# Kernel optimization log

Hardware: AMD Instinct MI355X
Metric: run time of the kernel (lower is better)

## Reference

```python
import jax, jax.numpy as jnp
import numpy as np

BLANK = 127
NEG = -1e30  # effective -inf that stays finite in fp32 arithmetic


def setup_inputs() -> dict:
    key = jax.random.key(0)
    k1, k2 = jax.random.split(key)
    outputs = jax.random.normal(k1, (64, 2048, 128), dtype=jnp.float32)
    # labels in [0, 127) -> never equal to blank (127)
    targets = jax.random.randint(k2, (64, 128), 0, BLANK)
    return {"outputs": outputs, "targets": targets}


def _ctc_loss(outputs, targets):
    # outputs: [B, T, V] logits, targets: [B, S] int labels (no blanks inside)
    B, T, V = outputs.shape
    S = targets.shape[1]
    L = 2 * S + 1  # extended label sequence length (blanks interleaved)

    log_probs = jax.nn.log_softmax(outputs, axis=2)  # [B, T, V]

    # extended labels: blank, y1, blank, y2, ..., blank
    ext = jnp.full((B, L), BLANK, dtype=targets.dtype)
    ext = ext.at[:, 1::2].set(targets)  # [B, L]

    # skip transition (l-2 -> l) allowed iff ext[l] != blank and ext[l] != ext[l-2]
    skip = jnp.concatenate(
        [jnp.zeros((B, 2), dtype=bool),
         (ext[:, 2:] != BLANK) & (ext[:, 2:] != ext[:, :-2])],
        axis=1,
    )  # [B, L]

    # gather per-step log-probs of extended labels: [B, T, L] -> [T, B, L]
    lp_ext = jnp.take_along_axis(log_probs, ext[:, None, :], axis=2)
    lp_ext = jnp.swapaxes(lp_ext, 0, 1)

    # alpha init at t=0: only states 0 (blank) and 1 (first label) reachable
    alpha0 = jnp.full((B, L), NEG, dtype=log_probs.dtype)
    alpha0 = alpha0.at[:, 0].set(lp_ext[0, :, 0])
    alpha0 = alpha0.at[:, 1].set(lp_ext[0, :, 1])

    neg1 = jnp.full((B, 1), NEG, dtype=log_probs.dtype)
    neg2 = jnp.full((B, 2), NEG, dtype=log_probs.dtype)

    def step(alpha, lp):
        s1 = jnp.concatenate([neg1, alpha[:, :-1]], axis=1)
        s2 = jnp.concatenate([neg2, alpha[:, :-2]], axis=1)
        s2 = jnp.where(skip, s2, NEG)
        alpha = lp + jnp.logaddexp(jnp.logaddexp(alpha, s1), s2)
        return alpha, None

    alphaT, _ = jax.lax.scan(step, alpha0, lp_ext[1:])

    # P(targets | outputs) ends in last blank or last label
    loss_b = -jnp.logaddexp(alphaT[:, L - 1], alphaT[:, L - 2])  # [B]

    # zero_infinity=True: unreachable paths -> zero loss
    loss_b = jnp.where(loss_b > 1e29, 0.0, loss_b)

    # reduction='mean': divide each loss by its target length, then batch-mean
    tl = jnp.sum(targets != BLANK, axis=1).astype(loss_b.dtype)
    return jnp.mean(loss_b / jnp.maximum(tl, 1.0))


def reference(outputs, targets):
    return _ctc_loss(outputs, targets)
```

## Files before the change

kernel.cpp:

```cpp
#include <hip/hip_runtime.h>
#include <stdint.h>


#define B_ 64
#define T_ 2048
#define V_ 128
#define S_ 128
#define BLANK 127
#define NCH 512
#define DEPTH 32
#define INFLT 28

__device__ __forceinline__ void glds16(const void* gsrc, void* lds) {
  __builtin_amdgcn_global_load_lds(
      (const __attribute__((address_space(1))) uint32_t*)gsrc,
      (__attribute__((address_space(3))) uint32_t*)lds, 16, 0, 0);
}

__global__ __launch_bounds__(256) void lse_kernel(const float* __restrict__ outp,
                                                  float2* __restrict__ lse2) {
  const float L2E = 1.4426950408889634f;
  int gtid = blockIdx.x * 256 + threadIdx.x;
  int wave = gtid >> 6;
  int lane = threadIdx.x & 63;
  long row = (long)wave * 2 + (lane >> 5);
  const float4 x = *(const float4*)(outp + row * V_ + (long)(lane & 31) * 4);
  float ex = exp2f(x.x * L2E), ey = exp2f(x.y * L2E);
  float ez = exp2f(x.z * L2E), ew = exp2f(x.w * L2E);
  float s = (ex + ey) + (ez + ew);
#pragma unroll
  for (int o = 1; o <= 16; o <<= 1) s += __shfl_xor(s, o);
  float bx = __shfl(x.w, (lane < 32) ? 31 : 63);
  if ((lane & 31) == 0) {
    float l2s = log2f(s);
    lse2[row] = make_float2(l2s, exp2f(fmaf(bx, L2E, -l2s)));
  }
}

__global__ __launch_bounds__(64) void ctc_alpha(const float* __restrict__ x,
                                                const float2* __restrict__ lse2,
                                                const int* __restrict__ tgt,
                                                float* __restrict__ lossb) {
  __shared__ __align__(16) float2 lp_s[T_];
  __shared__ __align__(16) float ring[DEPTH * 512];
  const float L2E = 1.4426950408889634f;
  const int b = blockIdx.x;
  const int k = threadIdx.x;

  const int2 tg = ((const int2*)(tgt + b * S_))[k];
  const int t1p = __shfl_up(tg.y, 1);
  const bool skip0 = (k > 0) && (tg.x != t1p);
  const bool skip1 = (tg.y != tg.x);
  const int tl = __popcll(__ballot(tg.x != BLANK)) + __popcll(__ballot(tg.y != BLANK));

  const float* lpsrc = (const float*)(lse2 + (long)b * T_);
#pragma unroll
  for (int i = 0; i < 16; ++i)
    glds16(lpsrc + i * 256 + k * 4, (float*)lp_s + i * 256);
  const float* xb = x + (long)b * T_ * V_;
  for (int i = 0; i < INFLT; ++i) {
    glds16(xb + i * 512 + k * 4, &ring[i * 512]);
    glds16(xb + i * 512 + 256 + k * 4, &ring[i * 512 + 256]);
  }
  asm volatile("s_waitcnt vmcnt(0)" ::: "memory");
  __builtin_amdgcn_sched_barrier(0);

  float fx0 = ring[0 * 128 + tg.x], fy0 = ring[0 * 128 + tg.y];
  float fx1 = ring[1 * 128 + tg.x], fy1 = ring[1 * 128 + tg.y];
  float fx2 = ring[2 * 128 + tg.x], fy2 = ring[2 * 128 + tg.y];
  float fx3 = ring[3 * 128 + tg.x], fy3 = ring[3 * 128 + tg.y];
  float2 lq0 = lp_s[0], lq1 = lp_s[1], lq2 = lp_s[2], lq3 = lp_s[3];

  float a0 = 0.f, a1 = 0.f, a2 = 0.f, a3 = 0.f, a4 = 0.f;
  float adj = 1.0f;
  int P = 0;

#define SUBSTEP(FX, FY, LQ) do {                                    \
    float p0 = exp2f(fmaf((FX), L2E, -(LQ).x));                     \
    float p1 = exp2f(fmaf((FY), L2E, -(LQ).x));                     \
    float pB = (LQ).y;                                              \
    float s1r = __shfl_up(a3, 1);                                   \
    float s1v = (k == 0) ? 0.f : s1r * adj;                         \
    float na0 = pB * (a0 + s1v);                                    \
    float na1 = p0 * (a1 + a0 + (skip0 ? s1v : 0.f));               \
    float na2 = pB * (a2 + a1);                                     \
    float na3 = p1 * (a3 + a2 + (skip1 ? a1 : 0.f));                \
    float na4 = pB * (a4 + a3);                                     \
    a4 = (k == 63) ? na4 : 0.f;                                     \
    a0 = na0; a1 = na1; a2 = na2; a3 = na3;                         \
  } while (0)

  int ws = INFLT % DEPTH, cn = INFLT;
  for (int c = 0; c < NCH; ++c) {
    glds16(xb + (long)cn * 512 + k * 4, &ring[ws * 512]);
    glds16(xb + (long)cn * 512 + 256 + k * 4, &ring[ws * 512 + 256]);
    asm volatile("s_waitcnt vmcnt(54)" ::: "memory");
    __builtin_amdgcn_sched_barrier(0);
    const int r2 = ((c + 1) & (DEPTH - 1)) * 512;
    const int li = (4 * (c + 1)) & (T_ - 1);
    float gx0 = ring[r2 + tg.x],       gy0 = ring[r2 + tg.y];
    float gx1 = ring[r2 + 128 + tg.x], gy1 = ring[r2 + 128 + tg.y];
    float gx2 = ring[r2 + 256 + tg.x], gy2 = ring[r2 + 256 + tg.y];
    float gx3 = ring[r2 + 384 + tg.x], gy3 = ring[r2 + 384 + tg.y];
    float2 mq0 = lp_s[li], mq1 = lp_s[li + 1];
    float2 mq2 = lp_s[li + 2], mq3 = lp_s[li + 3];
    if (c == 0) {
      a0 = (k == 0) ? lq0.y : 0.f;
      a1 = (k == 0) ? exp2f(fmaf(fx0, L2E, -lq0.x)) : 0.f;
      SUBSTEP(fx1, fy1, lq1); SUBSTEP(fx2, fy2, lq2); SUBSTEP(fx3, fy3, lq3);
    } else {
      SUBSTEP(fx0, fy0, lq0); SUBSTEP(fx1, fy1, lq1);
      SUBSTEP(fx2, fy2, lq2); SUBSTEP(fx3, fy3, lq3);
    }
    float ml = fmaxf(fmaxf(a0, a1), fmaxf(fmaxf(a2, a3), a4));
    int Plo = __shfl_up(P, 1);
    bool dead = (ml == 0.0f);
    int e = (int)((__float_as_uint(ml) >> 23) & 255) - 127;
    float sc = dead ? 1.0f : __uint_as_float((uint32_t)(127 - e) << 23);
    a0 *= sc; a1 *= sc; a2 *= sc; a3 *= sc; a4 *= sc;
    P = dead ? Plo : (P + e);
    int Pl2 = __shfl_up(P, 1);
    adj = ldexpf(1.0f, Pl2 - P);
    fx0 = gx0; fy0 = gy0; fx1 = gx1; fy1 = gy1;
    fx2 = gx2; fy2 = gy2; fx3 = gx3; fy3 = gy3;
    lq0 = mq0; lq1 = mq1; lq2 = mq2; lq3 = mq3;
    ++cn; if (cn == NCH) cn = 0;
    ++ws; if (ws == DEPTH) ws = 0;
  }
#undef SUBSTEP

  if (k == 63) {
    float aE = a3 + a4;
    float lb = -(logf(aE) + (float)P * 0.6931471805599453f);
    if (!(lb < 1e29f)) lb = 0.0f;
    lossb[b] = lb / fmaxf((float)tl, 1.0f);
  }
}

__global__ __launch_bounds__(64) void finalize_kernel(const float* __restrict__ lossb,
                                                      float* __restrict__ outv) {
  int k = threadIdx.x;
  float v = lossb[k];
#pragma unroll
  for (int o = 1; o < 64; o <<= 1) v += __shfl_xor(v, o);
  if (k == 0) outv[0] = v * (1.0f / B_);
}

extern "C" void kernel_launch(void* const* d_in, const int* in_sizes, int n_in,
                              void* d_out, int out_size, void* d_ws, size_t ws_size,
                              hipStream_t stream) {
  const float* outputs = (const float*)d_in[0];
  const int* targets = (const int*)d_in[1];
  float2* lse2 = (float2*)d_ws;
  float* lossb = (float*)((char*)d_ws + (size_t)B_ * T_ * sizeof(float2));
  float* outv = (float*)d_out;

  lse_kernel<<<16384, 256, 0, stream>>>(outputs, lse2);
  ctc_alpha<<<B_, 64, 0, stream>>>(outputs, lse2, targets, lossb);
  finalize_kernel<<<1, 64, 0, stream>>>(lossb, outv);
}
```

Measured before the change: 319.8 us.

## Replace LDS ring buffer with register-prefetched slots and bpermute gathers

The CTC alpha kernel no longer stages logits and LSE values through an LDS ring filled by global_load_lds. Instead each thread loads chunk rows straight into eight rotating register slots, eight chunks ahead, and gathers the target-label logits across lanes with ds_bpermute. The recursion is also trimmed: the k==0 and k==63 selects are folded into adj and the skip multipliers, and renormalisation now runs every other chunk instead of every chunk. The aim is to remove LDS traffic, waitcnt stalls and per-step work from the serial critical path. The cost is much higher register pressure, and less frequent rescaling, which raises the risk of fp32 underflow.

Result: slower. 405.4 us (+26.8%).

```diff
diff --git a/kernel.cpp b/kernel.cpp
--- a/kernel.cpp
+++ b/kernel.cpp
@@ -8,14 +8,6 @@
 #define S_ 128
 #define BLANK 127
 #define NCH 512
-#define DEPTH 32
-#define INFLT 28
-
-__device__ __forceinline__ void glds16(const void* gsrc, void* lds) {
-  __builtin_amdgcn_global_load_lds(
-      (const __attribute__((address_space(1))) uint32_t*)gsrc,
-      (__attribute__((address_space(3))) uint32_t*)lds, 16, 0, 0);
-}
 
 __global__ __launch_bounds__(256) void lse_kernel(const float* __restrict__ outp,
                                                   float2* __restrict__ lse2) {
@@ -37,97 +29,122 @@
   }
 }
 
+struct Slot {
+  float2 r0, r1, r2, r3;
+  float4 la, lb;
+};
+
 __global__ __launch_bounds__(64) void ctc_alpha(const float* __restrict__ x,
                                                 const float2* __restrict__ lse2,
                                                 const int* __restrict__ tgt,
                                                 float* __restrict__ lossb) {
-  __shared__ __align__(16) float2 lp_s[T_];
-  __shared__ __align__(16) float ring[DEPTH * 512];
   const float L2E = 1.4426950408889634f;
   const int b = blockIdx.x;
   const int k = threadIdx.x;
+  const bool kz = (k == 0);
 
   const int2 tg = ((const int2*)(tgt + b * S_))[k];
   const int t1p = __shfl_up(tg.y, 1);
-  const bool skip0 = (k > 0) && (tg.x != t1p);
-  const bool skip1 = (tg.y != tg.x);
+  const float sk0 = (k > 0 && tg.x != t1p) ? 1.0f : 0.0f;
+  const float sk1 = (tg.y != tg.x) ? 1.0f : 0.0f;
   const int tl = __popcll(__ballot(tg.x != BLANK)) + __popcll(__ballot(tg.y != BLANK));
+  const int ad0 = (tg.x >> 1) << 2, ad1 = (tg.y >> 1) << 2;
+  const bool cs0 = tg.x & 1, cs1 = tg.y & 1;
 
-  const float* lpsrc = (const float*)(lse2 + (long)b * T_);
-#pragma unroll
-  for (int i = 0; i < 16; ++i)
-    glds16(lpsrc + i * 256 + k * 4, (float*)lp_s + i * 256);
-  const float* xb = x + (long)b * T_ * V_;
-  for (int i = 0; i < INFLT; ++i) {
-    glds16(xb + i * 512 + k * 4, &ring[i * 512]);
-    glds16(xb + i * 512 + 256 + k * 4, &ring[i * 512 + 256]);
-  }
-  asm volatile("s_waitcnt vmcnt(0)" ::: "memory");
-  __builtin_amdgcn_sched_barrier(0);
+  const float2* xb2 = (const float2*)(x + (long)b * T_ * V_);
+  const float2* lse2b = lse2 + (long)b * T_;
 
-  float fx0 = ring[0 * 128 + tg.x], fy0 = ring[0 * 128 + tg.y];
-  float fx1 = ring[1 * 128 + tg.x], fy1 = ring[1 * 128 + tg.y];
-  float fx2 = ring[2 * 128 + tg.x], fy2 = ring[2 * 128 + tg.y];
-  float fx3 = ring[3 * 128 + tg.x], fy3 = ring[3 * 128 + tg.y];
-  float2 lq0 = lp_s[0], lq1 = lp_s[1], lq2 = lp_s[2], lq3 = lp_s[3];
-
+  Slot s0_, s1_, s2_, s3_, s4_, s5_, s6_, s7_;
+  float p00, p01, p10, p11, p20, p21, p30, p31;
   float a0 = 0.f, a1 = 0.f, a2 = 0.f, a3 = 0.f, a4 = 0.f;
-  float adj = 1.0f;
+  float adj = kz ? 0.f : 1.0f;
   int P = 0;
 
-#define SUBSTEP(FX, FY, LQ) do {                                    \
-    float p0 = exp2f(fmaf((FX), L2E, -(LQ).x));                     \
-    float p1 = exp2f(fmaf((FY), L2E, -(LQ).x));                     \
-    float pB = (LQ).y;                                              \
-    float s1r = __shfl_up(a3, 1);                                   \
-    float s1v = (k == 0) ? 0.f : s1r * adj;                         \
-    float na0 = pB * (a0 + s1v);                                    \
-    float na1 = p0 * (a1 + a0 + (skip0 ? s1v : 0.f));               \
-    float na2 = pB * (a2 + a1);                                     \
-    float na3 = p1 * (a3 + a2 + (skip1 ? a1 : 0.f));                \
-    float na4 = pB * (a4 + a3);                                     \
-    a4 = (k == 63) ? na4 : 0.f;                                     \
-    a0 = na0; a1 = na1; a2 = na2; a3 = na3;                         \
+#define LOADSLOT(S, CC) do {                                          \
+    const float2* rp_ = xb2 + (CC) * 256;                             \
+    (S).r0 = rp_[k]; (S).r1 = rp_[64 + k];                            \
+    (S).r2 = rp_[128 + k]; (S).r3 = rp_[192 + k];                     \
+    const float4* lp_ = (const float4*)(lse2b + (CC) * 4);            \
+    (S).la = lp_[0]; (S).lb = lp_[1];                                 \
   } while (0)
 
-  int ws = INFLT % DEPTH, cn = INFLT;
-  for (int c = 0; c < NCH; ++c) {
-    glds16(xb + (long)cn * 512 + k * 4, &ring[ws * 512]);
-    glds16(xb + (long)cn * 512 + 256 + k * 4, &ring[ws * 512 + 256]);
-    asm volatile("s_waitcnt vmcnt(54)" ::: "memory");
-    __builtin_amdgcn_sched_barrier(0);
-    const int r2 = ((c + 1) & (DEPTH - 1)) * 512;
-    const int li = (4 * (c + 1)) & (T_ - 1);
-    float gx0 = ring[r2 + tg.x],       gy0 = ring[r2 + tg.y];
-    float gx1 = ring[r2 + 128 + tg.x], gy1 = ring[r2 + 128 + tg.y];
-    float gx2 = ring[r2 + 256 + tg.x], gy2 = ring[r2 + 256 + tg.y];
-    float gx3 = ring[r2 + 384 + tg.x], gy3 = ring[r2 + 384 + tg.y];
-    float2 mq0 = lp_s[li], mq1 = lp_s[li + 1];
-    float2 mq2 = lp_s[li + 2], mq3 = lp_s[li + 3];
-    if (c == 0) {
-      a0 = (k == 0) ? lq0.y : 0.f;
-      a1 = (k == 0) ? exp2f(fmaf(fx0, L2E, -lq0.x)) : 0.f;
-      SUBSTEP(fx1, fy1, lq1); SUBSTEP(fx2, fy2, lq2); SUBSTEP(fx3, fy3, lq3);
-    } else {
-      SUBSTEP(fx0, fy0, lq0); SUBSTEP(fx1, fy1, lq1);
-      SUBSTEP(fx2, fy2, lq2); SUBSTEP(fx3, fy3, lq3);
-    }
-    float ml = fmaxf(fmaxf(a0, a1), fmaxf(fmaxf(a2, a3), a4));
-    int Plo = __shfl_up(P, 1);
-    bool dead = (ml == 0.0f);
-    int e = (int)((__float_as_uint(ml) >> 23) & 255) - 127;
-    float sc = dead ? 1.0f : __uint_as_float((uint32_t)(127 - e) << 23);
-    a0 *= sc; a1 *= sc; a2 *= sc; a3 *= sc; a4 *= sc;
-    P = dead ? Plo : (P + e);
-    int Pl2 = __shfl_up(P, 1);
-    adj = ldexpf(1.0f, Pl2 - P);
-    fx0 = gx0; fy0 = gy0; fx1 = gx1; fy1 = gy1;
-    fx2 = gx2; fy2 = gy2; fx3 = gx3; fy3 = gy3;
-    lq0 = mq0; lq1 = mq1; lq2 = mq2; lq3 = mq3;
-    ++cn; if (cn == NCH) cn = 0;
-    ++ws; if (ws == DEPTH) ws = 0;
+#define GS(RR, AD, ODD) ({                                            \
+    int h_ = __builtin_amdgcn_ds_bpermute((AD), __float_as_int((RR).x)); \
+    int g_ = __builtin_amdgcn_ds_bpermute((AD), __float_as_int((RR).y)); \
+    __int_as_float((ODD) ? g_ : h_); })
+
+#define GATHER(S) do {                                                \
+    float v_;                                                         \
+    v_ = GS((S).r0, ad0, cs0); p00 = exp2f(fmaf(v_, L2E, -(S).la.x)); \
+    v_ = GS((S).r0, ad1, cs1); p01 = exp2f(fmaf(v_, L2E, -(S).la.x)); \
+    v_ = GS((S).r1, ad0, cs0); p10 = exp2f(fmaf(v_, L2E, -(S).la.z)); \
+    v_ = GS((S).r1, ad1, cs1); p11 = exp2f(fmaf(v_, L2E, -(S).la.z)); \
+    v_ = GS((S).r2, ad0, cs0); p20 = exp2f(fmaf(v_, L2E, -(S).lb.x)); \
+    v_ = GS((S).r2, ad1, cs1); p21 = exp2f(fmaf(v_, L2E, -(S).lb.x)); \
+    v_ = GS((S).r3, ad0, cs0); p30 = exp2f(fmaf(v_, L2E, -(S).lb.z)); \
+    v_ = GS((S).r3, ad1, cs1); p31 = exp2f(fmaf(v_, L2E, -(S).lb.z)); \
+  } while (0)
+
+#define SUBSTEP(P0, P1, PB) do {                                      \
+    float s1r = __shfl_up(a3, 1);                                     \
+    float s1v = s1r * adj;                                            \
+    float na0 = (PB) * (a0 + s1v);                                    \
+    float na1 = (P0) * (a1 + fmaf(sk0, s1v, a0));                     \
+    float na2 = (PB) * (a2 + a1);                                     \
+    float na3 = (P1) * (a3 + fmaf(sk1, a1, a2));                      \
+    float na4 = (PB) * (a4 + a3);                                     \
+    a0 = na0; a1 = na1; a2 = na2; a3 = na3; a4 = na4;                 \
+  } while (0)
+
+#define RESCALE do {                                                  \
+    float ml = fmaxf(fmaxf(a0, a1), fmaxf(fmaxf(a2, a3), a4));        \
+    int Plo = __shfl_up(P, 1);                                        \
+    bool dead = (ml == 0.0f);                                         \
+    int e = (int)((__float_as_uint(ml) >> 23) & 255) - 127;           \
+    float sc = dead ? 1.0f : __uint_as_float((uint32_t)(127 - e) << 23); \
+    a0 *= sc; a1 *= sc; a2 *= sc; a3 *= sc; a4 *= sc;                 \
+    P = dead ? Plo : (P + e);                                         \
+    int Pl2 = __shfl_up(P, 1);                                        \
+    adj = ldexpf(kz ? 0.f : 1.0f, Pl2 - P);                           \
+  } while (0)
+
+#define BODY(SJ, SN, BASE, JOFF, INIT) do {                           \
+    const int c_ = (BASE) + (JOFF);                                   \
+    if ((INIT) && c_ == 0) {      \
+      a0 = kz ? (SJ).la.y : 0.f;                                      \
+      a1 = kz ? p00 : 0.f;                                            \
+    } else {                                                          \
+      SUBSTEP(p00, p01, (SJ).la.y);                                   \
+    }                                                                 \
+    SUBSTEP(p10, p11, (SJ).la.w);                                     \
+    SUBSTEP(p20, p21, (SJ).lb.y);                                     \
+    SUBSTEP(p30, p31, (SJ).lb.w);                                     \
+    if ((JOFF) & 1) RESCALE;                                          \
+    GATHER(SN);                       \
+    LOADSLOT(SJ, (c_ + 8) & (NCH - 1));    \
+  } while (0)
+
+  LOADSLOT(s0_, 0); LOADSLOT(s1_, 1); LOADSLOT(s2_, 2); LOADSLOT(s3_, 3);
+  LOADSLOT(s4_, 4); LOADSLOT(s5_, 5); LOADSLOT(s6_, 6); LOADSLOT(s7_, 7);
+  GATHER(s0_);
+
+  for (int blk = 0; blk < NCH / 8; ++blk) {
+    const int base = blk << 3;
+    BODY(s0_, s1_, base, 0, 1);
+    BODY(s1_, s2_, base, 1, 0);
+    BODY(s2_, s3_, base, 2, 0);
+    BODY(s3_, s4_, base, 3, 0);
+    BODY(s4_, s5_, base, 4, 0);
+    BODY(s5_, s6_, base, 5, 0);
+    BODY(s6_, s7_, base, 6, 0);
+    BODY(s7_, s0_, base, 7, 0);
   }
+#undef BODY
+#undef RESCALE
 #undef SUBSTEP
+#undef GATHER
+#undef GS
+#undef LOADSLOT
 
   if (k == 63) {
     float aE = a3 + a4;
```
